# Kernel tuning notes

Measured on AMD Instinct MI355X. Metric: run time of the kernel, lower is better.

## Reference

```python
import jax, jax.numpy as jnp
import numpy as np

B, D = 16, 8192
CH = 32
N_BLOCKS = 24
DILATIONS = [2 ** i for i in range(8)] * 3  # 3 stacks of 8 layers


def _causal_conv(x, W, b, dilation):
    # x: (B, Cin, L); W: (Cout, Cin, K). Causal = left-pad (K-1)*dilation only,
    # which equals torch's symmetric-pad-then-slice-right trick.
    pad = (W.shape[-1] - 1) * dilation
    y = jax.lax.conv_general_dilated(
        x, W, window_strides=(1,), padding=[(pad, 0)],
        rhs_dilation=(dilation,), dimension_numbers=('NCH', 'OIH', 'NCH'))
    return y + b[None, :, None]


def setup_inputs() -> dict:
    key = jax.random.key(0)
    ks = jax.random.split(key, 13)
    s = 0.1  # keep activations in a sane range
    return {
        'x': jax.random.normal(ks[0], (B, D), jnp.float32),
        'W0': jax.random.normal(ks[1], (CH, 1, 2), jnp.float32) * s,
        'b0': jax.random.normal(ks[2], (CH,), jnp.float32) * s,
        'Wd': jax.random.normal(ks[3], (N_BLOCKS, 2 * CH, CH, 2), jnp.float32) * s,
        'bd': jax.random.normal(ks[4], (N_BLOCKS, 2 * CH), jnp.float32) * s,
        'W1': jax.random.normal(ks[5], (N_BLOCKS, CH, CH), jnp.float32) * s,
        'b1': jax.random.normal(ks[6], (N_BLOCKS, CH), jnp.float32) * s,
        'Wf': jax.random.normal(ks[7], (CH, CH), jnp.float32) * s,
        'bf': jax.random.normal(ks[8], (CH,), jnp.float32) * s,
        'fW1': jax.random.normal(ks[9], (64, CH * 4), jnp.float32) * s,
        'fb1': jax.random.normal(ks[10], (64,), jnp.float32) * s,
        'fW2': jax.random.normal(ks[11], (10, 64), jnp.float32) * s,
        'fb2': jax.random.normal(ks[12], (10,), jnp.float32) * s,
    }


def reference(x, W0, b0, Wd, bd, W1, b1, Wf, bf, fW1, fb1, fW2, fb2):
    h = _causal_conv(x[:, None, :], W0, b0, 1)  # (B, 32, L)
    skip_sum = jnp.zeros_like(h)
    for i, dil in enumerate(DILATIONS):
        z = _causal_conv(h, Wd[i], bd[i], dil)          # (B, 64, L)
        f, g = jnp.split(z, 2, axis=1)
        gated = jnp.tanh(f) * jax.nn.sigmoid(g)          # (B, 32, L)
        skip = jnp.einsum('oc,bcl->bol', W1[i], gated) + b1[i][None, :, None]
        h = h + skip                                     # residual (dropout = eval identity)
        skip_sum = skip_sum + skip                       # sum of stacked skips
    y = jax.nn.relu(skip_sum)
    y = jnp.einsum('oc,bcl->bol', Wf, y) + bf[None, :, None]
    y = jax.nn.relu(y)
    # AdaptiveMaxPool1d(4): L divisible by 4 -> max over contiguous chunks
    Bc, C, L = y.shape
    y = y.reshape(Bc, C, 4, L // 4).max(axis=-1)         # (B, 32, 4)
    y = y.reshape(Bc, C * 4)
    y = jax.nn.relu(y @ fW1.T + fb1)
    return y @ fW2.T + fb2
```

## Files before the change

### kernel.cpp

```cpp
#include <hip/hip_runtime.h>
#include <hip/hip_bf16.h>

#define BATCH 16
#define SEQ 8192
#define CH 32
#define NB 24

typedef __attribute__((ext_vector_type(8))) short short8;
typedef __attribute__((ext_vector_type(4))) short short4v;
typedef __attribute__((ext_vector_type(4))) float f32x4;

__device__ __forceinline__ unsigned short f2bf(float x) {
    __hip_bfloat16 b = __float2bfloat16(x);
    unsigned short u;
    __builtin_memcpy(&u, &b, 2);
    return u;
}
__device__ __forceinline__ float bf2f(unsigned short h) {
    return __uint_as_float(((unsigned int)h) << 16);
}
__device__ __forceinline__ float rcp_fast(float x) { return __builtin_amdgcn_rcpf(x); }

__device__ __forceinline__ float gate_fn(float f, float g) {
    float ef = __expf(-2.0f * fabsf(f));
    float eg = __expf(-g);
    float num = 1.0f - ef;
    float den = (1.0f + ef) * (1.0f + eg);
    return copysignf(num * rcp_fast(den), f);
}

__device__ __forceinline__ void split2(float v, unsigned short& h, unsigned short& l) {
    h = f2bf(v);
    l = f2bf(v - bf2f(h));
}

__global__ __launch_bounds__(256) void k_prep(const float* __restrict__ Wd,
                                              const float* __restrict__ bd,
                                              const float* __restrict__ W1,
                                              const float* __restrict__ b1,
                                              unsigned short* __restrict__ stream,
                                              float* __restrict__ pooled) {
    int i = blockIdx.x;
    int tid = threadIdx.x;
    int l = tid & 63, q4 = tid >> 6;
    int p = l & 15, h4 = l >> 4;
    const float* wd  = Wd + (size_t)i * 64 * 64;
    const float* w1  = W1 + (size_t)i * 1024;
    const float* bdp = bd + (size_t)i * 64;
    const float* b1p = b1 + (size_t)i * 32;
    unsigned short* out = stream + (size_t)i * (28672 / 2);

    for (int g = blockIdx.x * 256 + tid; g < BATCH * CH * 4; g += NB * 256)
        pooled[g] = 0.0f;

    {
        int rt = q4;
        int is_g = (rt >= 2) ? 32 : 0;
        int ch = 8 * (p >> 2) + 4 * (rt & 1) + (p & 3);
        int row = ch + is_g;
        for (int q = 0; q < 2; ++q) {
            int slot = rt * 2 + q;
            for (int j = 0; j < 8; ++j) {
                int k = 32 * q + 8 * h4 + j;
                int c = k & 31, tap = k >> 5;
                float w = wd[row * 64 + c * 2 + tap];
                unsigned short hi = f2bf(w);
                out[(size_t)slot * 512 + l * 8 + j] = hi;
                out[(size_t)(8 + slot) * 512 + l * 8 + j] = f2bf(w - bf2f(hi));
            }
        }
    }
    if (q4 < 2) {
        int rt2 = q4;
        for (int j = 0; j < 8; ++j) {
            int o = 16 * rt2 + p, c = 8 * h4 + j;
            float w = w1[o * 32 + c];
            unsigned short hi = f2bf(w);
            out[(size_t)(16 + rt2) * 512 + l * 8 + j] = hi;
            out[(size_t)(18 + rt2) * 512 + l * 8 + j] = f2bf(w - bf2f(hi));
        }
    }
    float* outf = (float*)stream + (size_t)i * (28672 / 4);
    if (q4 == 2) {
        for (int rt = 0; rt < 4; ++rt) {
            int is_g = (rt >= 2) ? 32 : 0;
            for (int r = 0; r < 4; ++r)
                outf[(size_t)(20 + rt) * 256 + l * 4 + r] =
                    bdp[8 * h4 + 4 * (rt & 1) + r + is_g];
        }
    }
    if (q4 == 3) {
        for (int rt2 = 0; rt2 < 2; ++rt2)
            for (int r = 0; r < 4; ++r)
                outf[(size_t)(24 + rt2) * 256 + l * 4 + r] = b1p[16 * rt2 + 4 * h4 + r];
    }
}

__global__ __launch_bounds__(1024, 4) void k_stack(
        const unsigned short* __restrict__ hin_hi,
        const unsigned short* __restrict__ hin_lo,
        unsigned short* __restrict__ hout_hi,
        unsigned short* __restrict__ hout_lo,
        const float* __restrict__ x,
        const float* __restrict__ W0,
        const float* __restrict__ b0,
        const float* __restrict__ Wf,
        const float* __restrict__ bf,
        float* __restrict__ pooled,
        const unsigned short* __restrict__ wstream,
        int stack) {
    __shared__ __align__(16) unsigned short lhi[768][40];
    __shared__ __align__(16) unsigned short llo[768][40];

    int tid = threadIdx.x;
    int lane = tid & 63, wave = tid >> 6;
    int p = lane & 15, h4 = lane >> 4;
    int bb = blockIdx.x >> 4;
    int T0 = (blockIdx.x & 15) * 512;
    bool first = (stack == 0);
    bool last  = (stack == 2);

    const unsigned short* pin_hi = hin_hi + (size_t)bb * SEQ * CH;
    const unsigned short* pin_lo = hin_lo + (size_t)bb * SEQ * CH;
    unsigned short* pout_hi = hout_hi + (size_t)bb * SEQ * CH;
    unsigned short* pout_lo = hout_lo + (size_t)bb * SEQ * CH;
    const float* px = x + (size_t)bb * SEQ;

    const short8 zero8 = {0, 0, 0, 0, 0, 0, 0, 0};

    if (tid < 768) {
        int i = tid;
        int t = T0 - 256 + i;
        if (first) {
            if (t >= 0) {
                float xt = px[t];
                float xm = (t > 0) ? px[t - 1] : 0.0f;
#pragma unroll
                for (int c = 0; c < CH; ++c) {
                    float v = W0[c * 2] * xm + W0[c * 2 + 1] * xt + b0[c];
                    unsigned short hh, ll;
                    split2(v, hh, ll);
                    lhi[i][c] = hh;
                    llo[i][c] = ll;
                }
            } else {
#pragma unroll
                for (int k = 0; k < 4; ++k) {
                    *(short8*)&lhi[i][8 * k] = zero8;
                    *(short8*)&llo[i][8 * k] = zero8;
                }
            }
        } else {
            if (t >= 0) {
                const unsigned short* sh = pin_hi + (size_t)t * CH;
                const unsigned short* sl = pin_lo + (size_t)t * CH;
#pragma unroll
                for (int k = 0; k < 4; ++k) {
                    *(short8*)&lhi[i][8 * k] = *(const short8*)(sh + 8 * k);
                    *(short8*)&llo[i][8 * k] = *(const short8*)(sl + 8 * k);
                }
            } else {
#pragma unroll
                for (int k = 0; k < 4; ++k) {
                    *(short8*)&lhi[i][8 * k] = zero8;
                    *(short8*)&llo[i][8 * k] = zero8;
                }
            }
        }
    }
    __syncthreads();

#pragma unroll 1
    for (int l = 0; l < 8; ++l) {
        int dil = 1 << l;
        const unsigned short* frag = wstream + (size_t)(8 * stack + l) * 14336;
        const short8* fs = (const short8*)frag;
        short8 Ah[4][2], Al[4][2], Sh[2], Sl[2];
#pragma unroll
        for (int rt = 0; rt < 4; ++rt)
#pragma unroll
            for (int q = 0; q < 2; ++q) {
                Ah[rt][q] = fs[(rt * 2 + q) * 64 + lane];
                Al[rt][q] = fs[(8 + rt * 2 + q) * 64 + lane];
            }
#pragma unroll
        for (int rt2 = 0; rt2 < 2; ++rt2) {
            Sh[rt2] = fs[(16 + rt2) * 64 + lane];
            Sl[rt2] = fs[(18 + rt2) * 64 + lane];
        }
        const f32x4* ff = (const f32x4*)frag;
        f32x4 bFG[4], bS[2];
#pragma unroll
        for (int rt = 0; rt < 4; ++rt) bFG[rt] = ff[(20 + rt) * 64 + lane];
#pragma unroll
        for (int rt2 = 0; rt2 < 2; ++rt2) bS[rt2] = ff[(24 + rt2) * 64 + lane];

        f32x4 hnew[3][2];

#pragma unroll
        for (int s6 = 0; s6 < 3; ++s6) {
            int tpos = wave * 48 + s6 * 16 + p;
            int tq = tpos - dil;
            bool ok = (T0 - 256 + tq >= 0);
            int tqc = (tq > 0) ? tq : 0;

            short8 bh1 = *(const short8*)&lhi[tpos][8 * h4];
            short8 bl1 = *(const short8*)&llo[tpos][8 * h4];
            short8 bh0 = *(const short8*)&lhi[tqc][8 * h4];
            short8 bl0 = *(const short8*)&llo[tqc][8 * h4];
            if (!ok) { bh0 = zero8; bl0 = zero8; }

            short8 Bgh, Bgl;
#pragma unroll
            for (int half = 0; half < 2; ++half) {
                f32x4 af = bFG[half];
                f32x4 ag = bFG[half + 2];
                af = __builtin_amdgcn_mfma_f32_16x16x32_bf16(Ah[half][0], bh0, af, 0, 0, 0);
                ag = __builtin_amdgcn_mfma_f32_16x16x32_bf16(Ah[half + 2][0], bh0, ag, 0, 0, 0);
                af = __builtin_amdgcn_mfma_f32_16x16x32_bf16(Ah[half][1], bh1, af, 0, 0, 0);
                ag = __builtin_amdgcn_mfma_f32_16x16x32_bf16(Ah[half + 2][1], bh1, ag, 0, 0, 0);
                af = __builtin_amdgcn_mfma_f32_16x16x32_bf16(Ah[half][0], bl0, af, 0, 0, 0);
                ag = __builtin_amdgcn_mfma_f32_16x16x32_bf16(Ah[half + 2][0], bl0, ag, 0, 0, 0);
                af = __builtin_amdgcn_mfma_f32_16x16x32_bf16(Ah[half][1], bl1, af, 0, 0, 0);
                ag = __builtin_amdgcn_mfma_f32_16x16x32_bf16(Ah[half + 2][1], bl1, ag, 0, 0, 0);
                af = __builtin_amdgcn_mfma_f32_16x16x32_bf16(Al[half][0], bh0, af, 0, 0, 0);
                ag = __builtin_amdgcn_mfma_f32_16x16x32_bf16(Al[half + 2][0], bh0, ag, 0, 0, 0);
                af = __builtin_amdgcn_mfma_f32_16x16x32_bf16(Al[half][1], bh1, af, 0, 0, 0);
                ag = __builtin_amdgcn_mfma_f32_16x16x32_bf16(Al[half + 2][1], bh1, ag, 0, 0, 0);
#pragma unroll
                for (int r = 0; r < 4; ++r) {
                    float gated = gate_fn(af[r], ag[r]);
                    unsigned short hh, ll;
                    split2(gated, hh, ll);
                    Bgh[4 * half + r] = (short)hh;
                    Bgl[4 * half + r] = (short)ll;
                }
            }

            f32x4 sacc[2];
#pragma unroll
            for (int rt2 = 0; rt2 < 2; ++rt2) {
                f32x4 a = bS[rt2];
                a = __builtin_amdgcn_mfma_f32_16x16x32_bf16(Sh[rt2], Bgh, a, 0, 0, 0);
                a = __builtin_amdgcn_mfma_f32_16x16x32_bf16(Sh[rt2], Bgl, a, 0, 0, 0);
                a = __builtin_amdgcn_mfma_f32_16x16x32_bf16(Sl[rt2], Bgh, a, 0, 0, 0);
                sacc[rt2] = a;
            }

#pragma unroll
            for (int rt2 = 0; rt2 < 2; ++rt2) {
                int ch = 16 * rt2 + 4 * h4;
                short4v hh = *(const short4v*)&lhi[tpos][ch];
                short4v hl = *(const short4v*)&llo[tpos][ch];
                f32x4 hv;
#pragma unroll
                for (int r = 0; r < 4; ++r)
                    hv[r] = bf2f((unsigned short)hh[r]) + bf2f((unsigned short)hl[r]);
                hnew[s6][rt2] = hv + sacc[rt2];
            }
        }
        __syncthreads();

#pragma unroll
        for (int s6 = 0; s6 < 3; ++s6) {
            int tpos = wave * 48 + s6 * 16 + p;
#pragma unroll
            for (int rt2 = 0; rt2 < 2; ++rt2) {
                __align__(8) unsigned short oh[4], ol[4];
#pragma unroll
                for (int r = 0; r < 4; ++r)
                    split2(hnew[s6][rt2][r], oh[r], ol[r]);
                int ch = 16 * rt2 + 4 * h4;
                *(short4v*)&lhi[tpos][ch] = *(const short4v*)oh;
                *(short4v*)&llo[tpos][ch] = *(const short4v*)ol;
            }
        }
        __syncthreads();
    }

    if (!last) {
        if (tid < 512) {
            int i = 256 + tid;
            int t = T0 + tid;
            unsigned short* dh = pout_hi + (size_t)t * CH;
            unsigned short* dl = pout_lo + (size_t)t * CH;
#pragma unroll
            for (int k = 0; k < 4; ++k) {
                *(short8*)(dh + 8 * k) = *(const short8*)&lhi[i][8 * k];
                *(short8*)(dl + 8 * k) = *(const short8*)&llo[i][8 * k];
            }
        }
    } else {
        float* red = (float*)&lhi[0][0];
        int q = (blockIdx.x & 15) >> 2;
        if (tid < 512) {
            int i = 256 + tid;
            int t = T0 + tid;
            float xt = px[t];
            float xm = (t > 0) ? px[t - 1] : 0.0f;

            float r[CH];
#pragma unroll
            for (int c = 0; c < CH; ++c) {
                float h0 = W0[c * 2] * xm + W0[c * 2 + 1] * xt + b0[c];
                float hf = bf2f(lhi[i][c]) + bf2f(llo[i][c]);
                r[c] = fmaxf(hf - h0, 0.0f);
            }
            float y[CH];
#pragma unroll 1
            for (int o = 0; o < CH; ++o) {
                const float* w = Wf + o * CH;
                float a0 = bf[o], a1 = 0.0f, a2 = 0.0f, a3 = 0.0f;
#pragma unroll
                for (int c = 0; c < CH; c += 4) {
                    a0 += w[c + 0] * r[c + 0];
                    a1 += w[c + 1] * r[c + 1];
                    a2 += w[c + 2] * r[c + 2];
                    a3 += w[c + 3] * r[c + 3];
                }
                y[o] = fmaxf((a0 + a1) + (a2 + a3), 0.0f);
            }
#pragma unroll
            for (int o = 0; o < CH; ++o) {
#pragma unroll
                for (int off = 32; off >= 1; off >>= 1)
                    y[o] = fmaxf(y[o], __shfl_xor(y[o], off));
            }
            if (lane == 0) {
#pragma unroll
                for (int o = 0; o < CH; ++o) red[wave * CH + o] = y[o];
            }
        }
        __syncthreads();
        if (tid < CH) {
            float m = red[tid];
#pragma unroll
            for (int w8 = 1; w8 < 8; ++w8) m = fmaxf(m, red[w8 * CH + tid]);
            atomicMax((unsigned int*)&pooled[bb * (CH * 4) + tid * 4 + q],
                      __float_as_uint(m));
        }
    }
}

__global__ __launch_bounds__(1024) void k_final2(const float* __restrict__ pooled,
                                                 const float* __restrict__ fW1,
                                                 const float* __restrict__ fb1,
                                                 const float* __restrict__ fW2,
                                                 const float* __restrict__ fb2,
                                                 float* __restrict__ out) {
    __shared__ float y1[BATCH * 64];
    int tid = threadIdx.x;
    int b = tid >> 6, o = tid & 63;
    float acc = fb1[o];
#pragma unroll
    for (int j = 0; j < 128; ++j) acc += fW1[o * 128 + j] * pooled[b * 128 + j];
    y1[b * 64 + o] = fmaxf(acc, 0.0f);
    __syncthreads();
    if (tid < BATCH * 10) {
        int bb = tid / 10, o2 = tid % 10;
        float a2 = fb2[o2];
#pragma unroll
        for (int j = 0; j < 64; ++j) a2 += fW2[o2 * 64 + j] * y1[bb * 64 + j];
        out[bb * 10 + o2] = a2;
    }
}

extern "C" void kernel_launch(void* const* d_in, const int* in_sizes, int n_in,
                              void* d_out, int out_size, void* d_ws, size_t ws_size,
                              hipStream_t stream) {
    const float* x   = (const float*)d_in[0];
    const float* W0  = (const float*)d_in[1];
    const float* b0  = (const float*)d_in[2];
    const float* Wd  = (const float*)d_in[3];
    const float* bd  = (const float*)d_in[4];
    const float* W1  = (const float*)d_in[5];
    const float* b1  = (const float*)d_in[6];
    const float* Wf  = (const float*)d_in[7];
    const float* bf  = (const float*)d_in[8];
    const float* fW1 = (const float*)d_in[9];
    const float* fb1 = (const float*)d_in[10];
    const float* fW2 = (const float*)d_in[11];
    const float* fb2 = (const float*)d_in[12];
    float* out = (float*)d_out;

    const size_t HS = (size_t)BATCH * SEQ * CH;
    unsigned short* hiA = (unsigned short*)d_ws;
    unsigned short* loA = hiA + HS;
    unsigned short* hiB = loA + HS;
    unsigned short* loB = hiB + HS;
    unsigned short* wstream = loB + HS;
    float* pooled = (float*)(wstream + (size_t)NB * 14336);

    k_prep<<<NB, 256, 0, stream>>>(Wd, bd, W1, b1, wstream, pooled);

    k_stack<<<256, 1024, 0, stream>>>(hiA, loA, hiB, loB, x, W0, b0, Wf, bf,
                                      pooled, wstream, 0);
    k_stack<<<256, 1024, 0, stream>>>(hiB, loB, hiA, loA, x, W0, b0, Wf, bf,
                                      pooled, wstream, 1);
    k_stack<<<256, 1024, 0, stream>>>(hiA, loA, hiB, loB, x, W0, b0, Wf, bf,
                                      pooled, wstream, 2);

    k_final2<<<1, 1024, 0, stream>>>(pooled, fW1, fb1, fW2, fb2, out);
}
```

Before: 322.1 us.

## Stage per-layer weight fragments in LDS and simplify bf16 conversion

Each layer's weight and bias fragments are now copied cooperatively into a shared-memory buffer, and every wave reads them from there instead of loading them per wave from global memory. The next layer's weights are staged after the h write-back, before the existing barrier. The bf16 round-to-nearest is hand-coded, and the low residual is truncated rather than rounded, which saves instructions but slightly changes the numerics of the hi/lo split. The causal mask check is also simplified to apply only in the first time tile. The cost is roughly 26 KB more LDS per block, which may reduce occupancy, and the weight copy sits on the critical path between layers.

```diff
diff --git a/kernel.cpp b/kernel.cpp
--- a/kernel.cpp
+++ b/kernel.cpp
@@ -1,5 +1,4 @@
 #include <hip/hip_runtime.h>
-#include <hip/hip_bf16.h>
 
 #define BATCH 16
 #define SEQ 8192
@@ -9,12 +8,11 @@
 typedef __attribute__((ext_vector_type(8))) short short8;
 typedef __attribute__((ext_vector_type(4))) short short4v;
 typedef __attribute__((ext_vector_type(4))) float f32x4;
+typedef __attribute__((ext_vector_type(4))) unsigned int uint4v;
 
 __device__ __forceinline__ unsigned short f2bf(float x) {
-    __hip_bfloat16 b = __float2bfloat16(x);
-    unsigned short u;
-    __builtin_memcpy(&u, &b, 2);
-    return u;
+    unsigned int u = __float_as_uint(x);
+    return (unsigned short)((u + 0x7FFFu + ((u >> 16) & 1u)) >> 16);
 }
 __device__ __forceinline__ float bf2f(unsigned short h) {
     return __uint_as_float(((unsigned int)h) << 16);
@@ -31,7 +29,7 @@
 
 __device__ __forceinline__ void split2(float v, unsigned short& h, unsigned short& l) {
     h = f2bf(v);
-    l = f2bf(v - bf2f(h));
+    l = (unsigned short)(__float_as_uint(v - bf2f(h)) >> 16);
 }
 
 __global__ __launch_bounds__(256) void k_prep(const float* __restrict__ Wd,
@@ -96,6 +94,8 @@
     }
 }
 
+#define WSLOTS 13312
+
 __global__ __launch_bounds__(1024, 4) void k_stack(
         const unsigned short* __restrict__ hin_hi,
         const unsigned short* __restrict__ hin_lo,
@@ -111,6 +111,7 @@
         int stack) {
     __shared__ __align__(16) unsigned short lhi[768][40];
     __shared__ __align__(16) unsigned short llo[768][40];
+    __shared__ __align__(16) unsigned short wbuf[WSLOTS];
 
     int tid = threadIdx.x;
     int lane = tid & 63, wave = tid >> 6;
@@ -127,6 +128,7 @@
     const float* px = x + (size_t)bb * SEQ;
 
     const short8 zero8 = {0, 0, 0, 0, 0, 0, 0, 0};
+    const unsigned short* wsbase = wstream + (size_t)(8 * stack) * 14336;
 
     if (tid < 768) {
         int i = tid;
@@ -168,13 +170,17 @@
             }
         }
     }
+    {
+        const uint4v* src = (const uint4v*)wsbase;
+        uint4v* dst = (uint4v*)wbuf;
+        for (int j = tid; j < WSLOTS / 8; j += 1024) dst[j] = src[j];
+    }
     __syncthreads();
 
 #pragma unroll 1
     for (int l = 0; l < 8; ++l) {
         int dil = 1 << l;
-        const unsigned short* frag = wstream + (size_t)(8 * stack + l) * 14336;
-        const short8* fs = (const short8*)frag;
+        const short8* fs = (const short8*)wbuf;
         short8 Ah[4][2], Al[4][2], Sh[2], Sl[2];
 #pragma unroll
         for (int rt = 0; rt < 4; ++rt)
@@ -188,7 +194,7 @@
             Sh[rt2] = fs[(16 + rt2) * 64 + lane];
             Sl[rt2] = fs[(18 + rt2) * 64 + lane];
         }
-        const f32x4* ff = (const f32x4*)frag;
+        const f32x4* ff = (const f32x4*)wbuf;
         f32x4 bFG[4], bS[2];
 #pragma unroll
         for (int rt = 0; rt < 4; ++rt) bFG[rt] = ff[(20 + rt) * 64 + lane];
@@ -201,14 +207,15 @@
         for (int s6 = 0; s6 < 3; ++s6) {
             int tpos = wave * 48 + s6 * 16 + p;
             int tq = tpos - dil;
-            bool ok = (T0 - 256 + tq >= 0);
             int tqc = (tq > 0) ? tq : 0;
 
             short8 bh1 = *(const short8*)&lhi[tpos][8 * h4];
             short8 bl1 = *(const short8*)&llo[tpos][8 * h4];
             short8 bh0 = *(const short8*)&lhi[tqc][8 * h4];
             short8 bl0 = *(const short8*)&llo[tqc][8 * h4];
-            if (!ok) { bh0 = zero8; bl0 = zero8; }
+            if (T0 == 0) {
+                if (tq < 256) { bh0 = zero8; bl0 = zero8; }
+            }
 
             short8 Bgh, Bgl;
 #pragma unroll
@@ -274,6 +281,11 @@
                 *(short4v*)&lhi[tpos][ch] = *(const short4v*)oh;
                 *(short4v*)&llo[tpos][ch] = *(const short4v*)ol;
             }
+        }
+        if (l < 7) {
+            const uint4v* src = (const uint4v*)(wsbase + (size_t)(l + 1) * 14336);
+            uint4v* dst = (uint4v*)wbuf;
+            for (int j = tid; j < WSLOTS / 8; j += 1024) dst[j] = src[j];
         }
         __syncthreads();
     }
```

Result: slower. 608.3 us (+88.8%).
